# Kernel optimization log

Measured on AMD Instinct MI355X. Metric: run time of the kernel, lower is better.

Reference implementation:

```python
import jax, jax.numpy as jnp
import numpy as np

IN_CH, KEY_CH, VAL_CH, HEADS = 64, 32, 32, 2


def setup_inputs() -> dict:
    key = jax.random.key(0)
    ks = jax.random.split(key, 9)
    n, d, h, w = 2, 16, 128, 128
    sc_in = 1.0 / np.sqrt(IN_CH)
    sc_v = 1.0 / np.sqrt(VAL_CH)
    return {
        "x": jax.random.normal(ks[0], (n, IN_CH, d, h, w), dtype=jnp.float32),
        "Wk": jax.random.normal(ks[1], (KEY_CH, IN_CH), dtype=jnp.float32) * sc_in,
        "bk": jax.random.normal(ks[2], (KEY_CH,), dtype=jnp.float32) * 0.01,
        "Wq": jax.random.normal(ks[3], (KEY_CH, IN_CH), dtype=jnp.float32) * sc_in,
        "bq": jax.random.normal(ks[4], (KEY_CH,), dtype=jnp.float32) * 0.01,
        "Wv": jax.random.normal(ks[5], (VAL_CH, IN_CH), dtype=jnp.float32) * sc_in,
        "bv": jax.random.normal(ks[6], (VAL_CH,), dtype=jnp.float32) * 0.01,
        "Wr": jax.random.normal(ks[7], (IN_CH, VAL_CH), dtype=jnp.float32) * sc_v,
        "br": jax.random.normal(ks[8], (IN_CH,), dtype=jnp.float32) * 0.01,
    }


def reference(x, Wk, bk, Wq, bq, Wv, bv, Wr, br):
    n, C, d, h, w = x.shape
    S = d * h * w
    H = HEADS
    hk = KEY_CH // H   # per-head key channels
    hv = VAL_CH // H   # per-head value channels
    xf = x.reshape(n, C, S)
    # 1x1x1 Conv3d == channel-wise linear projection
    k = jnp.einsum('oi,nis->nos', Wk, xf) + bk[:, None]
    q = jnp.einsum('oi,nis->nos', Wq, xf) + bq[:, None]
    v = jnp.einsum('oi,nis->nos', Wv, xf) + bv[:, None]
    # heads vectorized: key softmax over sequence S, query softmax over head channels
    k = jax.nn.softmax(k.reshape(n, H, hk, S), axis=-1)
    q = jax.nn.softmax(q.reshape(n, H, hk, S), axis=2)
    v = v.reshape(n, H, hv, S)
    # context = K @ V^T : [n, H, hk, hv]  (linear attention, O(S) not O(S^2))
    ctx = jnp.einsum('nhks,nhvs->nhkv', k, v)
    # attended = context^T @ Q : [n, H, hv, S]
    att = jnp.einsum('nhkv,nhks->nhvs', ctx, q).reshape(n, VAL_CH, S)
    out = jnp.einsum('oi,nis->nos', Wr, att) + br[:, None]
    return out.reshape(n, C, d, h, w) + x
```

## Files before the change

### kernel.cpp

```cpp
#include <hip/hip_runtime.h>
#include <hip/hip_bf16.h>

#define SEQ 262144
#define PAD 260

__device__ __forceinline__ float bflo(unsigned u) { return __uint_as_float(u << 16); }
__device__ __forceinline__ float bfhi(unsigned u) { return __uint_as_float(u & 0xffff0000u); }
__device__ __forceinline__ unsigned short f2bf(float f) {
    unsigned b = __float_as_uint(f);
    b += 0x7fffu + ((b >> 16) & 1u);
    return (unsigned short)(b >> 16);
}

__global__ __launch_bounds__(256) void nl_k1(
    const float* __restrict__ x,
    const float* __restrict__ Wk, const float* __restrict__ bk,
    const float* __restrict__ Wv, const float* __restrict__ bv,
    float* __restrict__ ctx_g, float* __restrict__ z_g)
{
    __shared__ unsigned short EKs[32 * PAD];
    __shared__ unsigned short Vs [32 * PAD];

    const int tid   = threadIdx.x;
    const int b     = blockIdx.x;
    const int n     = b >> 8;
    const int chunk = b & 255;
    const float* xn = x + (size_t)n * 64 * SEQ;

    const int rk0 = tid >> 4, rv0 = tid & 15;
    const int rk1 = rk0 + 16, rv1 = rv0 + 16;
    float acc0 = 0.f, acc1 = 0.f, zacc = 0.f;
    const int zrow = tid >> 3;
    const int zseg = (tid & 7) * 32;

    for (int tile = 0; tile < 4; ++tile) {
        const int s = chunk * 1024 + tile * 256 + tid;

        float xr[64];
        #pragma unroll
        for (int c = 0; c < 64; ++c) xr[c] = xn[(size_t)c * SEQ + s];

        float ek[32], vv[32];
        #pragma unroll
        for (int o = 0; o < 32; ++o) {
            const float4* wk4 = reinterpret_cast<const float4*>(Wk + o * 64);
            const float4* wv4 = reinterpret_cast<const float4*>(Wv + o * 64);
            float ak = bk[o], av = bv[o];
            #pragma unroll
            for (int c4 = 0; c4 < 16; ++c4) {
                const float4 wa = wk4[c4];
                const float4 wb = wv4[c4];
                ak = fmaf(wa.x, xr[c4*4+0], ak); av = fmaf(wb.x, xr[c4*4+0], av);
                ak = fmaf(wa.y, xr[c4*4+1], ak); av = fmaf(wb.y, xr[c4*4+1], av);
                ak = fmaf(wa.z, xr[c4*4+2], ak); av = fmaf(wb.z, xr[c4*4+2], av);
                ak = fmaf(wa.w, xr[c4*4+3], ak); av = fmaf(wb.w, xr[c4*4+3], av);
            }
            ek[o] = __expf(ak);
            vv[o] = av;
        }

        __syncthreads();
        #pragma unroll
        for (int o = 0; o < 32; ++o) {
            EKs[o * PAD + tid] = f2bf(ek[o]);
            Vs [o * PAD + tid] = f2bf(vv[o]);
        }
        __syncthreads();

        for (int t = 0; t < 256; t += 4) {
            const uint2 ka = *reinterpret_cast<const uint2*>(&EKs[rk0 * PAD + t]);
            const uint2 va = *reinterpret_cast<const uint2*>(&Vs [rv0 * PAD + t]);
            const uint2 kb = *reinterpret_cast<const uint2*>(&EKs[rk1 * PAD + t]);
            const uint2 vb = *reinterpret_cast<const uint2*>(&Vs [rv1 * PAD + t]);
            acc0 = fmaf(bflo(ka.x), bflo(va.x), acc0);
            acc0 = fmaf(bfhi(ka.x), bfhi(va.x), acc0);
            acc0 = fmaf(bflo(ka.y), bflo(va.y), acc0);
            acc0 = fmaf(bfhi(ka.y), bfhi(va.y), acc0);
            acc1 = fmaf(bflo(kb.x), bflo(vb.x), acc1);
            acc1 = fmaf(bfhi(kb.x), bfhi(vb.x), acc1);
            acc1 = fmaf(bflo(kb.y), bflo(vb.y), acc1);
            acc1 = fmaf(bfhi(kb.y), bfhi(vb.y), acc1);
        }
        for (int t = zseg; t < zseg + 32; t += 4) {
            const uint2 p = *reinterpret_cast<const uint2*>(&EKs[zrow * PAD + t]);
            zacc += bflo(p.x) + bfhi(p.x) + bflo(p.y) + bfhi(p.y);
        }
    }

    atomicAdd(&ctx_g[n * 512 + tid],       acc0);
    atomicAdd(&ctx_g[n * 512 + 256 + tid], acc1);

    zacc += __shfl_xor(zacc, 1, 8);
    zacc += __shfl_xor(zacc, 2, 8);
    zacc += __shfl_xor(zacc, 4, 8);
    if ((tid & 7) == 0) atomicAdd(&z_g[n * 32 + zrow], zacc);
}

__global__ __launch_bounds__(256) void nl_k2(
    const float* __restrict__ x,
    const float* __restrict__ Wq, const float* __restrict__ bq,
    const float* __restrict__ Wr, const float* __restrict__ br,
    const float* __restrict__ ctx_g, const float* __restrict__ z_g,
    float* __restrict__ out)
{
    __shared__ float ctxn[512];
    const int tid = threadIdx.x;
    const int b   = blockIdx.x;
    const int n   = b >> 10;
    const int s   = (b & 1023) * 256 + tid;

    ctxn[tid]       = ctx_g[n * 512 + tid]       / z_g[n * 32 + (tid >> 4)];
    ctxn[tid + 256] = ctx_g[n * 512 + 256 + tid] / z_g[n * 32 + 16 + (tid >> 4)];
    __syncthreads();

    const float* xn = x + (size_t)n * 64 * SEQ;
    float xr[64];
    #pragma unroll
    for (int c = 0; c < 64; ++c) xr[c] = xn[(size_t)c * SEQ + s];

    float ql[32];
    #pragma unroll
    for (int o = 0; o < 32; ++o) {
        const float4* w4 = reinterpret_cast<const float4*>(Wq + o * 64);
        float a = bq[o];
        #pragma unroll
        for (int c4 = 0; c4 < 16; ++c4) {
            const float4 w = w4[c4];
            a = fmaf(w.x, xr[c4*4+0], a);
            a = fmaf(w.y, xr[c4*4+1], a);
            a = fmaf(w.z, xr[c4*4+2], a);
            a = fmaf(w.w, xr[c4*4+3], a);
        }
        ql[o] = a;
    }

    float att[32];
    #pragma unroll
    for (int h = 0; h < 2; ++h) {
        float m = ql[h*16];
        #pragma unroll
        for (int j = 1; j < 16; ++j) m = fmaxf(m, ql[h*16 + j]);
        float eq[16]; float se = 0.f;
        #pragma unroll
        for (int j = 0; j < 16; ++j) { eq[j] = __expf(ql[h*16 + j] - m); se += eq[j]; }
        #pragma unroll
        for (int vc = 0; vc < 16; ++vc) att[h*16 + vc] = 0.f;
        #pragma unroll
        for (int kc = 0; kc < 16; ++kc) {
            const float e = eq[kc];
            #pragma unroll
            for (int vc = 0; vc < 16; ++vc)
                att[h*16 + vc] = fmaf(e, ctxn[h*256 + kc*16 + vc], att[h*16 + vc]);
        }
        const float inv = 1.f / se;
        #pragma unroll
        for (int vc = 0; vc < 16; ++vc) att[h*16 + vc] *= inv;
    }

    float* outn = out + (size_t)n * 64 * SEQ;
    #pragma unroll
    for (int c = 0; c < 64; ++c) {
        const float4* w4 = reinterpret_cast<const float4*>(Wr + c * 32);
        float a = br[c] + xr[c];
        #pragma unroll
        for (int j4 = 0; j4 < 8; ++j4) {
            const float4 w = w4[j4];
            a = fmaf(w.x, att[j4*4+0], a);
            a = fmaf(w.y, att[j4*4+1], a);
            a = fmaf(w.z, att[j4*4+2], a);
            a = fmaf(w.w, att[j4*4+3], a);
        }
        outn[(size_t)c * SEQ + s] = a;
    }
}

extern "C" void kernel_launch(void* const* d_in, const int* in_sizes, int n_in,
                              void* d_out, int out_size, void* d_ws, size_t ws_size,
                              hipStream_t stream) {
    const float* x  = (const float*)d_in[0];
    const float* Wk = (const float*)d_in[1];
    const float* bk = (const float*)d_in[2];
    const float* Wq = (const float*)d_in[3];
    const float* bq = (const float*)d_in[4];
    const float* Wv = (const float*)d_in[5];
    const float* bv = (const float*)d_in[6];
    const float* Wr = (const float*)d_in[7];
    const float* br = (const float*)d_in[8];
    float* out   = (float*)d_out;
    float* ctx_g = (float*)d_ws;
    float* z_g   = ctx_g + 1024;

    hipMemsetAsync(d_ws, 0, 1088 * sizeof(float), stream);
    nl_k1<<<dim3(512),  dim3(256), 0, stream>>>(x, Wk, bk, Wv, bv, ctx_g, z_g);
    nl_k2<<<dim3(2048), dim3(256), 0, stream>>>(x, Wq, bq, Wr, br, ctx_g, z_g, out);
}
```

Baseline: 630.7 us.

## Split key/value reduction across more blocks and precompute normalized context

The first kernel now processes one 256-position tile per block and launches 2048 blocks instead of looping over four tiles in 512 blocks. This raises parallelism and drops the inner-loop syncs. The cost is four times as many global atomics into the context accumulators. A new tiny kernel divides the context by the key normalizer once, so the second kernel reads the precomputed context through float4 global loads instead of rebuilding it in shared memory in every block.

New measurement: 518.6 us. 17.8% less time.

```diff
diff --git a/kernel.cpp b/kernel.cpp
--- a/kernel.cpp
+++ b/kernel.cpp
@@ -23,68 +23,65 @@
 
     const int tid   = threadIdx.x;
     const int b     = blockIdx.x;
-    const int n     = b >> 8;
-    const int chunk = b & 255;
+    const int n     = b >> 10;
+    const int chunk = b & 1023;
+    const int s     = chunk * 256 + tid;
     const float* xn = x + (size_t)n * 64 * SEQ;
+
+    float xr[64];
+    #pragma unroll
+    for (int c = 0; c < 64; ++c) xr[c] = xn[(size_t)c * SEQ + s];
+
+    float ek[32], vv[32];
+    #pragma unroll
+    for (int o = 0; o < 32; ++o) {
+        const float4* wk4 = reinterpret_cast<const float4*>(Wk + o * 64);
+        const float4* wv4 = reinterpret_cast<const float4*>(Wv + o * 64);
+        float ak = bk[o], av = bv[o];
+        #pragma unroll
+        for (int c4 = 0; c4 < 16; ++c4) {
+            const float4 wa = wk4[c4];
+            const float4 wb = wv4[c4];
+            ak = fmaf(wa.x, xr[c4*4+0], ak); av = fmaf(wb.x, xr[c4*4+0], av);
+            ak = fmaf(wa.y, xr[c4*4+1], ak); av = fmaf(wb.y, xr[c4*4+1], av);
+            ak = fmaf(wa.z, xr[c4*4+2], ak); av = fmaf(wb.z, xr[c4*4+2], av);
+            ak = fmaf(wa.w, xr[c4*4+3], ak); av = fmaf(wb.w, xr[c4*4+3], av);
+        }
+        ek[o] = __expf(ak);
+        vv[o] = av;
+    }
+
+    #pragma unroll
+    for (int o = 0; o < 32; ++o) {
+        EKs[o * PAD + tid] = f2bf(ek[o]);
+        Vs [o * PAD + tid] = f2bf(vv[o]);
+    }
+    __syncthreads();
 
     const int rk0 = tid >> 4, rv0 = tid & 15;
     const int rk1 = rk0 + 16, rv1 = rv0 + 16;
-    float acc0 = 0.f, acc1 = 0.f, zacc = 0.f;
+    float acc0 = 0.f, acc1 = 0.f;
+
+    for (int t = 0; t < 256; t += 4) {
+        const uint2 ka = *reinterpret_cast<const uint2*>(&EKs[rk0 * PAD + t]);
+        const uint2 va = *reinterpret_cast<const uint2*>(&Vs [rv0 * PAD + t]);
+        const uint2 kb = *reinterpret_cast<const uint2*>(&EKs[rk1 * PAD + t]);
+        const uint2 vb = *reinterpret_cast<const uint2*>(&Vs [rv1 * PAD + t]);
+        acc0 = fmaf(bflo(ka.x), bflo(va.x), acc0);
+        acc0 = fmaf(bfhi(ka.x), bfhi(va.x), acc0);
+        acc0 = fmaf(bflo(ka.y), bflo(va.y), acc0);
+        acc0 = fmaf(bfhi(ka.y), bfhi(va.y), acc0);
+        acc1 = fmaf(bflo(kb.x), bflo(vb.x), acc1);
+        acc1 = fmaf(bfhi(kb.x), bfhi(vb.x), acc1);
+        acc1 = fmaf(bflo(kb.y), bflo(vb.y), acc1);
+        acc1 = fmaf(bfhi(kb.y), bfhi(vb.y), acc1);
+    }
     const int zrow = tid >> 3;
     const int zseg = (tid & 7) * 32;
-
-    for (int tile = 0; tile < 4; ++tile) {
-        const int s = chunk * 1024 + tile * 256 + tid;
-
-        float xr[64];
-        #pragma unroll
-        for (int c = 0; c < 64; ++c) xr[c] = xn[(size_t)c * SEQ + s];
-
-        float ek[32], vv[32];
-        #pragma unroll
-        for (int o = 0; o < 32; ++o) {
-            const float4* wk4 = reinterpret_cast<const float4*>(Wk + o * 64);
-            const float4* wv4 = reinterpret_cast<const float4*>(Wv + o * 64);
-            float ak = bk[o], av = bv[o];
-            #pragma unroll
-            for (int c4 = 0; c4 < 16; ++c4) {
-                const float4 wa = wk4[c4];
-                const float4 wb = wv4[c4];
-                ak = fmaf(wa.x, xr[c4*4+0], ak); av = fmaf(wb.x, xr[c4*4+0], av);
-                ak = fmaf(wa.y, xr[c4*4+1], ak); av = fmaf(wb.y, xr[c4*4+1], av);
-                ak = fmaf(wa.z, xr[c4*4+2], ak); av = fmaf(wb.z, xr[c4*4+2], av);
-                ak = fmaf(wa.w, xr[c4*4+3], ak); av = fmaf(wb.w, xr[c4*4+3], av);
-            }
-            ek[o] = __expf(ak);
-            vv[o] = av;
-        }
-
-        __syncthreads();
-        #pragma unroll
-        for (int o = 0; o < 32; ++o) {
-            EKs[o * PAD + tid] = f2bf(ek[o]);
-            Vs [o * PAD + tid] = f2bf(vv[o]);
-        }
-        __syncthreads();
-
-        for (int t = 0; t < 256; t += 4) {
-            const uint2 ka = *reinterpret_cast<const uint2*>(&EKs[rk0 * PAD + t]);
-            const uint2 va = *reinterpret_cast<const uint2*>(&Vs [rv0 * PAD + t]);
-            const uint2 kb = *reinterpret_cast<const uint2*>(&EKs[rk1 * PAD + t]);
-            const uint2 vb = *reinterpret_cast<const uint2*>(&Vs [rv1 * PAD + t]);
-            acc0 = fmaf(bflo(ka.x), bflo(va.x), acc0);
-            acc0 = fmaf(bfhi(ka.x), bfhi(va.x), acc0);
-            acc0 = fmaf(bflo(ka.y), bflo(va.y), acc0);
-            acc0 = fmaf(bfhi(ka.y), bfhi(va.y), acc0);
-            acc1 = fmaf(bflo(kb.x), bflo(vb.x), acc1);
-            acc1 = fmaf(bfhi(kb.x), bfhi(vb.x), acc1);
-            acc1 = fmaf(bflo(kb.y), bflo(vb.y), acc1);
-            acc1 = fmaf(bfhi(kb.y), bfhi(vb.y), acc1);
-        }
-        for (int t = zseg; t < zseg + 32; t += 4) {
-            const uint2 p = *reinterpret_cast<const uint2*>(&EKs[zrow * PAD + t]);
-            zacc += bflo(p.x) + bfhi(p.x) + bflo(p.y) + bfhi(p.y);
-        }
+    float zacc = 0.f;
+    for (int t = zseg; t < zseg + 32; t += 4) {
+        const uint2 p = *reinterpret_cast<const uint2*>(&EKs[zrow * PAD + t]);
+        zacc += bflo(p.x) + bfhi(p.x) + bflo(p.y) + bfhi(p.y);
     }
 
     atomicAdd(&ctx_g[n * 512 + tid],       acc0);
@@ -96,22 +93,25 @@
     if ((tid & 7) == 0) atomicAdd(&z_g[n * 32 + zrow], zacc);
 }
 
+__global__ __launch_bounds__(512) void nl_k1b(
+    const float* __restrict__ ctx_g, const float* __restrict__ z_g,
+    float* __restrict__ ctxn)
+{
+    const int n = blockIdx.x;
+    const int e = threadIdx.x;
+    ctxn[n * 512 + e] = ctx_g[n * 512 + e] / z_g[n * 32 + (e >> 4)];
+}
+
 __global__ __launch_bounds__(256) void nl_k2(
     const float* __restrict__ x,
     const float* __restrict__ Wq, const float* __restrict__ bq,
     const float* __restrict__ Wr, const float* __restrict__ br,
-    const float* __restrict__ ctx_g, const float* __restrict__ z_g,
-    float* __restrict__ out)
+    const float* __restrict__ ctxn, float* __restrict__ out)
 {
-    __shared__ float ctxn[512];
     const int tid = threadIdx.x;
     const int b   = blockIdx.x;
     const int n   = b >> 10;
     const int s   = (b & 1023) * 256 + tid;
-
-    ctxn[tid]       = ctx_g[n * 512 + tid]       / z_g[n * 32 + (tid >> 4)];
-    ctxn[tid + 256] = ctx_g[n * 512 + 256 + tid] / z_g[n * 32 + 16 + (tid >> 4)];
-    __syncthreads();
 
     const float* xn = x + (size_t)n * 64 * SEQ;
     float xr[64];
@@ -134,6 +134,7 @@
         ql[o] = a;
     }
 
+    const float* ctxb = ctxn + n * 512;
     float att[32];
     #pragma unroll
     for (int h = 0; h < 2; ++h) {
@@ -148,9 +149,15 @@
         #pragma unroll
         for (int kc = 0; kc < 16; ++kc) {
             const float e = eq[kc];
+            const float4* cr = reinterpret_cast<const float4*>(ctxb + h*256 + kc*16);
             #pragma unroll
-            for (int vc = 0; vc < 16; ++vc)
-                att[h*16 + vc] = fmaf(e, ctxn[h*256 + kc*16 + vc], att[h*16 + vc]);
+            for (int v4 = 0; v4 < 4; ++v4) {
+                const float4 cv = cr[v4];
+                att[h*16 + v4*4+0] = fmaf(e, cv.x, att[h*16 + v4*4+0]);
+                att[h*16 + v4*4+1] = fmaf(e, cv.y, att[h*16 + v4*4+1]);
+                att[h*16 + v4*4+2] = fmaf(e, cv.z, att[h*16 + v4*4+2]);
+                att[h*16 + v4*4+3] = fmaf(e, cv.w, att[h*16 + v4*4+3]);
+            }
         }
         const float inv = 1.f / se;
         #pragma unroll
@@ -189,8 +196,10 @@
     float* out   = (float*)d_out;
     float* ctx_g = (float*)d_ws;
     float* z_g   = ctx_g + 1024;
+    float* ctxn  = z_g + 64;
 
     hipMemsetAsync(d_ws, 0, 1088 * sizeof(float), stream);
-    nl_k1<<<dim3(512),  dim3(256), 0, stream>>>(x, Wk, bk, Wv, bv, ctx_g, z_g);
-    nl_k2<<<dim3(2048), dim3(256), 0, stream>>>(x, Wq, bq, Wr, br, ctx_g, z_g, out);
-}
+    nl_k1 <<<dim3(2048), dim3(256), 0, stream>>>(x, Wk, bk, Wv, bv, ctx_g, z_g);
+    nl_k1b<<<dim3(2),    dim3(512), 0, stream>>>(ctx_g, z_g, ctxn);
+    nl_k2 <<<dim3(2048), dim3(256), 0, stream>>>(x, Wq, bq, Wr, br, ctxn, out);
+}
```
